# Optimization experiments

Measured on AMD Instinct MI355X. Metric: run time of the kernel, lower is better.

The kernel has to match this reference:

```python
import jax, jax.numpy as jnp
import numpy as np

H = 16  # num_heads


def setup_inputs() -> dict:
    key = jax.random.key(0)
    ks = jax.random.split(key, 12)
    B, L, E = 2, 2048, 1024
    s = 1.0 / np.sqrt(E)
    inp = {
        "query": jax.random.normal(ks[0], (B, L, E), jnp.float32),
        "key": jax.random.normal(ks[1], (B, L, E), jnp.float32),
        "value": jax.random.normal(ks[2], (B, L, E), jnp.float32),
        "Wq": jax.random.normal(ks[3], (E, E), jnp.float32) * s,
        "bq": jnp.zeros((E,), jnp.float32),
        "Wk": jax.random.normal(ks[4], (E, E), jnp.float32) * s,
        "bk": jnp.zeros((E,), jnp.float32),
        "Wv": jax.random.normal(ks[5], (E, E), jnp.float32) * s,
        "bv": jnp.zeros((E,), jnp.float32),
        "Wo": jax.random.normal(ks[6], (E, E), jnp.float32) * s,
        "bo": jnp.zeros((E,), jnp.float32),
    }
    return inp


def _split_heads(x, h):
    B, L, E = x.shape
    return x.reshape(B, L, h, E // h).transpose(0, 2, 1, 3)  # [B,h,L,d]


def reference(query, key, value, Wq, bq, Wk, bk, Wv, bv, Wo, bo):
    B, L, E = query.shape
    d = E // H
    q = _split_heads(query @ Wq.T + bq, H)
    k = _split_heads(key @ Wk.T + bk, H)
    v = _split_heads(value @ Wv.T + bv, H)
    scores = jnp.einsum("bhqd,bhkd->bhqk", q, k) / jnp.sqrt(jnp.float32(d))
    weights = jax.nn.softmax(scores, axis=-1)  # [B,h,L,L]
    # dropout is identity in eval mode (deterministic reference)
    Z = jnp.einsum("bhqk,bhkd->bhqd", weights, v)
    Z = Z.transpose(0, 2, 1, 3).reshape(B, L, E)
    out = Z @ Wo.T + bo
    return out, weights
```

## Files before the change

kernel.cpp:

```cpp
#include <hip/hip_runtime.h>

typedef _Float16 half8 __attribute__((ext_vector_type(8)));
typedef float floatx4 __attribute__((ext_vector_type(4)));

__device__ __forceinline__ int lds_off(int row, int chunk) {
    return row * 32 + ((chunk ^ (row & 3)) << 3);
}

template<bool A_F32, bool B_F32, int OUT_MODE>
__global__ __launch_bounds__(256) void gemm128(
    const void* __restrict__ Ap, int lda, long sAz,
    const void* __restrict__ Bp, int ldb, long sBz,
    const float* __restrict__ bias, float scale,
    void* __restrict__ Cp, long sCz, int K)
{
    __shared__ __align__(16) _Float16 sA[128 * 32];
    __shared__ __align__(16) _Float16 sB[128 * 32];

    const int t = threadIdx.x;
    const int tileN = blockIdx.x * 128;
    const int tileM = blockIdx.y * 128;
    const int z = blockIdx.z;

    const int srow = t >> 1, shalf = t & 1, c0 = shalf * 2;
    const int lane = t & 63, wave = t >> 6;
    const int wm = (wave >> 1) * 64, wn = (wave & 1) * 64;
    const int l15 = lane & 15, quad = lane >> 4;

    const char* Abase = (const char*)Ap + (long)z * sAz * (A_F32 ? 4 : 2);
    const char* Bbase = (const char*)Bp + (long)z * sBz * (B_F32 ? 4 : 2);

    floatx4 acc[4][4];
#pragma unroll
    for (int i = 0; i < 4; i++)
#pragma unroll
        for (int j = 0; j < 4; j++)
            acc[i][j] = (floatx4){0.f, 0.f, 0.f, 0.f};

    for (int k0 = 0; k0 < K; k0 += 32) {
        __syncthreads();
        if constexpr (A_F32) {
            const float* src = (const float*)Abase + (long)(tileM + srow) * lda + k0 + shalf * 16;
            float fx[16];
            *(float4*)(fx + 0)  = *(const float4*)(src + 0);
            *(float4*)(fx + 4)  = *(const float4*)(src + 4);
            *(float4*)(fx + 8)  = *(const float4*)(src + 8);
            *(float4*)(fx + 12) = *(const float4*)(src + 12);
            half8 h0, h1;
#pragma unroll
            for (int i = 0; i < 8; i++) { h0[i] = (_Float16)fx[i]; h1[i] = (_Float16)fx[8 + i]; }
            *(half8*)&sA[lds_off(srow, c0)]     = h0;
            *(half8*)&sA[lds_off(srow, c0 + 1)] = h1;
        } else {
            const _Float16* src = (const _Float16*)Abase + (long)(tileM + srow) * lda + k0 + shalf * 16;
            *(half8*)&sA[lds_off(srow, c0)]     = *(const half8*)(src);
            *(half8*)&sA[lds_off(srow, c0 + 1)] = *(const half8*)(src + 8);
        }
        if constexpr (B_F32) {
            const float* src = (const float*)Bbase + (long)(tileN + srow) * ldb + k0 + shalf * 16;
            float fx[16];
            *(float4*)(fx + 0)  = *(const float4*)(src + 0);
            *(float4*)(fx + 4)  = *(const float4*)(src + 4);
            *(float4*)(fx + 8)  = *(const float4*)(src + 8);
            *(float4*)(fx + 12) = *(const float4*)(src + 12);
            half8 h0, h1;
#pragma unroll
            for (int i = 0; i < 8; i++) { h0[i] = (_Float16)fx[i]; h1[i] = (_Float16)fx[8 + i]; }
            *(half8*)&sB[lds_off(srow, c0)]     = h0;
            *(half8*)&sB[lds_off(srow, c0 + 1)] = h1;
        } else {
            const _Float16* src = (const _Float16*)Bbase + (long)(tileN + srow) * ldb + k0 + shalf * 16;
            *(half8*)&sB[lds_off(srow, c0)]     = *(const half8*)(src);
            *(half8*)&sB[lds_off(srow, c0 + 1)] = *(const half8*)(src + 8);
        }
        __syncthreads();

        half8 af[4], bf[4];
#pragma unroll
        for (int i = 0; i < 4; i++) af[i] = *(const half8*)&sA[lds_off(wm + i * 16 + l15, quad)];
#pragma unroll
        for (int j = 0; j < 4; j++) bf[j] = *(const half8*)&sB[lds_off(wn + j * 16 + l15, quad)];
#pragma unroll
        for (int i = 0; i < 4; i++)
#pragma unroll
            for (int j = 0; j < 4; j++)
                acc[i][j] = __builtin_amdgcn_mfma_f32_16x16x32_f16(af[i], bf[j], acc[i][j], 0, 0, 0);
    }

#pragma unroll
    for (int i = 0; i < 4; i++) {
#pragma unroll
        for (int j = 0; j < 4; j++) {
#pragma unroll
            for (int r = 0; r < 4; r++) {
                const int row = tileM + wm + i * 16 + quad * 4 + r;
                const int col = tileN + wn + j * 16 + l15;
                float v = acc[i][j][r] * scale;
                if (bias) v += bias[col];
                if constexpr (OUT_MODE == 0) {
                    _Float16* dst = (_Float16*)Cp;
                    dst[(long)(((row >> 11) << 4) + (col >> 6)) * 131072 + (long)(row & 2047) * 64 + (col & 63)] = (_Float16)v;
                } else if constexpr (OUT_MODE == 1) {
                    _Float16* dst = (_Float16*)Cp;
                    dst[(long)(((row >> 11) << 4) + (col >> 6)) * 131072 + (long)(col & 63) * 2048 + (row & 2047)] = (_Float16)v;
                } else {
                    float* dst = (float*)Cp;
                    dst[(long)row * 1024 + col] = v;
                }
            }
        }
    }
}

__global__ __launch_bounds__(256, 2) void attn_fused(
    const _Float16* __restrict__ Q,
    const _Float16* __restrict__ K,
    const _Float16* __restrict__ Vt,
    float* __restrict__ W,
    _Float16* __restrict__ Z)
{
    __shared__ __align__(16) _Float16 sK[128 * 64];
    __shared__ __align__(16) _Float16 sV[64 * 128];
    __shared__ __align__(16) _Float16 sP[128 * 128];

    const int t = threadIdx.x;
    const int tileM = blockIdx.x * 128;
    const int bh = blockIdx.y;
    const int lane = t & 63, wave = t >> 6;
    const int l15 = lane & 15, quad = lane >> 4;
    const int wm = wave * 32;

    const _Float16* Qb = Q + (long)bh * 131072;
    const _Float16* Kb = K + (long)bh * 131072;
    const _Float16* Vb = Vt + (long)bh * 131072;
    float* Wb = W + (long)bh * 4194304;

    const int krow = t >> 1, khalf = t & 1;
    const int vrow = t >> 2, vq = t & 3;

    half8 qf[2][2];
#pragma unroll
    for (int i = 0; i < 2; i++)
#pragma unroll
        for (int kk = 0; kk < 2; kk++)
            qf[i][kk] = *(const half8*)(Qb + (long)(tileM + wm + i * 16 + l15) * 64 + kk * 32 + quad * 8);

    float m[2][4], l[2][4];
#pragma unroll
    for (int i = 0; i < 2; i++)
#pragma unroll
        for (int r = 0; r < 4; r++) { m[i][r] = -__builtin_inff(); l[i][r] = 0.f; }

    for (int kv = 0; kv < 2048; kv += 128) {
        __syncthreads();
        {
            const _Float16* src = Kb + (long)(kv + krow) * 64 + khalf * 32;
#pragma unroll
            for (int c = 0; c < 4; c++)
                *(half8*)&sK[krow * 64 + ((((khalf * 4 + c)) ^ (krow & 7)) << 3)] = *(const half8*)(src + c * 8);
        }
        __syncthreads();

        floatx4 acc[2][8];
#pragma unroll
        for (int i = 0; i < 2; i++)
#pragma unroll
            for (int j = 0; j < 8; j++) acc[i][j] = (floatx4){0.f, 0.f, 0.f, 0.f};

#pragma unroll
        for (int kk = 0; kk < 2; kk++) {
#pragma unroll
            for (int j = 0; j < 8; j++) {
                const int row = j * 16 + l15;
                half8 bf = *(const half8*)&sK[row * 64 + (((kk * 4 + quad) ^ (row & 7)) << 3)];
                acc[0][j] = __builtin_amdgcn_mfma_f32_16x16x32_f16(qf[0][kk], bf, acc[0][j], 0, 0, 0);
                acc[1][j] = __builtin_amdgcn_mfma_f32_16x16x32_f16(qf[1][kk], bf, acc[1][j], 0, 0, 0);
            }
        }

#pragma unroll
        for (int i = 0; i < 2; i++)
#pragma unroll
            for (int r = 0; r < 4; r++) {
                float tmax = acc[i][0][r];
#pragma unroll
                for (int j = 1; j < 8; j++) tmax = fmaxf(tmax, acc[i][j][r]);
#pragma unroll
                for (int off = 1; off < 16; off <<= 1) tmax = fmaxf(tmax, __shfl_xor(tmax, off));
                const float mn = fmaxf(m[i][r], tmax * 0.125f);
                const float corr = __expf(m[i][r] - mn);
                float ts = 0.f;
#pragma unroll
                for (int j = 0; j < 8; j++) ts += __expf(acc[i][j][r] * 0.125f - mn);
#pragma unroll
                for (int off = 1; off < 16; off <<= 1) ts += __shfl_xor(ts, off);
                l[i][r] = l[i][r] * corr + ts;
                m[i][r] = mn;
            }
    }

#pragma unroll
    for (int i = 0; i < 2; i++)
#pragma unroll
        for (int r = 0; r < 4; r++) l[i][r] = 1.f / l[i][r];

    floatx4 accz[2][4];
#pragma unroll
    for (int i = 0; i < 2; i++)
#pragma unroll
        for (int j = 0; j < 4; j++) accz[i][j] = (floatx4){0.f, 0.f, 0.f, 0.f};

    for (int kv = 0; kv < 2048; kv += 128) {
        __syncthreads();
        {
            const _Float16* src = Kb + (long)(kv + krow) * 64 + khalf * 32;
#pragma unroll
            for (int c = 0; c < 4; c++)
                *(half8*)&sK[krow * 64 + ((((khalf * 4 + c)) ^ (krow & 7)) << 3)] = *(const half8*)(src + c * 8);
            const _Float16* vsrc = Vb + (long)vrow * 2048 + kv;
#pragma unroll
            for (int c = 0; c < 4; c++) {
                const int ch = vq + c * 4;
                *(half8*)&sV[vrow * 128 + ((ch ^ (vrow & 15)) << 3)] = *(const half8*)(vsrc + ch * 8);
            }
        }
        __syncthreads();

        floatx4 acc[2][8];
#pragma unroll
        for (int i = 0; i < 2; i++)
#pragma unroll
            for (int j = 0; j < 8; j++) acc[i][j] = (floatx4){0.f, 0.f, 0.f, 0.f};

#pragma unroll
        for (int kk = 0; kk < 2; kk++) {
#pragma unroll
            for (int j = 0; j < 8; j++) {
                const int row = j * 16 + l15;
                half8 bf = *(const half8*)&sK[row * 64 + (((kk * 4 + quad) ^ (row & 7)) << 3)];
                acc[0][j] = __builtin_amdgcn_mfma_f32_16x16x32_f16(qf[0][kk], bf, acc[0][j], 0, 0, 0);
                acc[1][j] = __builtin_amdgcn_mfma_f32_16x16x32_f16(qf[1][kk], bf, acc[1][j], 0, 0, 0);
            }
        }

#pragma unroll
        for (int i = 0; i < 2; i++) {
#pragma unroll
            for (int r = 0; r < 4; r++) {
                const int q = wm + i * 16 + quad * 4 + r;
                float* wr = Wb + (long)(tileM + q) * 2048 + kv + l15;
                _Float16* sprow = &sP[q * 128 + (l15 & 7)];
                const int qx = q & 15;
                const int hi = l15 >> 3;
#pragma unroll
                for (int j = 0; j < 8; j++) {
                    const float p = __expf(acc[i][j][r] * 0.125f - m[i][r]) * l[i][r];
                    __builtin_nontemporal_store(p, wr + j * 16);
                    sprow[((j * 2 + hi) ^ qx) << 3] = (_Float16)p;
                }
            }
        }
        __syncthreads();

#pragma unroll
        for (int kk = 0; kk < 4; kk++) {
            half8 pf[2];
#pragma unroll
            for (int i = 0; i < 2; i++) {
                const int q = wm + i * 16 + l15;
                pf[i] = *(const half8*)&sP[q * 128 + (((kk * 4 + quad) ^ (q & 15)) << 3)];
            }
#pragma unroll
            for (int j = 0; j < 4; j++) {
                const int d = j * 16 + l15;
                half8 vf = *(const half8*)&sV[d * 128 + (((kk * 4 + quad) ^ (d & 15)) << 3)];
                accz[0][j] = __builtin_amdgcn_mfma_f32_16x16x32_f16(pf[0], vf, accz[0][j], 0, 0, 0);
                accz[1][j] = __builtin_amdgcn_mfma_f32_16x16x32_f16(pf[1], vf, accz[1][j], 0, 0, 0);
            }
        }
    }

    const int bb = bh >> 4, hd = bh & 15;
#pragma unroll
    for (int i = 0; i < 2; i++)
#pragma unroll
        for (int j = 0; j < 4; j++)
#pragma unroll
            for (int r = 0; r < 4; r++)
                Z[(long)(bb * 2048 + tileM + wm + i * 16 + quad * 4 + r) * 1024 + hd * 64 + j * 16 + l15] =
                    (_Float16)accz[i][j][r];
}

extern "C" void kernel_launch(void* const* d_in, const int* in_sizes, int n_in,
                              void* d_out, int out_size, void* d_ws, size_t ws_size,
                              hipStream_t stream) {
    (void)in_sizes; (void)n_in; (void)out_size; (void)ws_size;
    const float* query = (const float*)d_in[0];
    const float* key   = (const float*)d_in[1];
    const float* value = (const float*)d_in[2];
    const float* Wq = (const float*)d_in[3];
    const float* bq = (const float*)d_in[4];
    const float* Wk = (const float*)d_in[5];
    const float* bk = (const float*)d_in[6];
    const float* Wv = (const float*)d_in[7];
    const float* bv = (const float*)d_in[8];
    const float* Wo = (const float*)d_in[9];
    const float* bo = (const float*)d_in[10];

    _Float16* wsQ  = (_Float16*)d_ws;
    _Float16* wsK  = wsQ + 4194304;
    _Float16* wsVt = wsK + 4194304;
    _Float16* wsZ  = wsVt + 4194304;

    float* outF = (float*)d_out;
    float* Wgt  = outF + 4194304;

    dim3 blk(256);
    gemm128<true, true, 0><<<dim3(8, 32, 1), blk, 0, stream>>>(query, 1024, 0, Wq, 1024, 0, bq, 1.0f, wsQ, 0, 1024);
    gemm128<true, true, 0><<<dim3(8, 32, 1), blk, 0, stream>>>(key,   1024, 0, Wk, 1024, 0, bk, 1.0f, wsK, 0, 1024);
    gemm128<true, true, 1><<<dim3(8, 32, 1), blk, 0, stream>>>(value, 1024, 0, Wv, 1024, 0, bv, 1.0f, wsVt, 0, 1024);
    attn_fused<<<dim3(16, 32), blk, 0, stream>>>(wsQ, wsK, wsVt, Wgt, wsZ);
    gemm128<false, true, 2><<<dim3(8, 32, 1), blk, 0, stream>>>(wsZ, 1024, 0, Wo, 1024, 0, bo, 1.0f, outF, 0, 1024);
}
```

Before: 904.0 us.

## Prefetch next tiles into registers and batch QKV projections into one launch

```diff
diff --git a/kernel.cpp b/kernel.cpp
--- a/kernel.cpp
+++ b/kernel.cpp
@@ -1,18 +1,30 @@
 #include <hip/hip_runtime.h>
 
 typedef _Float16 half8 __attribute__((ext_vector_type(8)));
+typedef _Float16 half4 __attribute__((ext_vector_type(4)));
 typedef float floatx4 __attribute__((ext_vector_type(4)));
 
 __device__ __forceinline__ int lds_off(int row, int chunk) {
     return row * 32 + ((chunk ^ (row & 3)) << 3);
 }
 
-template<bool A_F32, bool B_F32, int OUT_MODE>
-__global__ __launch_bounds__(256) void gemm128(
-    const void* __restrict__ Ap, int lda, long sAz,
-    const void* __restrict__ Bp, int ldb, long sBz,
-    const float* __restrict__ bias, float scale,
-    void* __restrict__ Cp, long sCz, int K)
+__device__ __forceinline__ void ld16f(float* d, const float* s) {
+    *(float4*)(d + 0)  = *(const float4*)(s + 0);
+    *(float4*)(d + 4)  = *(const float4*)(s + 4);
+    *(float4*)(d + 8)  = *(const float4*)(s + 8);
+    *(float4*)(d + 12) = *(const float4*)(s + 12);
+}
+
+__device__ __forceinline__ void cvt16(half8& h0, half8& h1, const float* f) {
+#pragma unroll
+    for (int i = 0; i < 8; i++) { h0[i] = (_Float16)f[i]; h1[i] = (_Float16)f[8 + i]; }
+}
+
+__global__ __launch_bounds__(256) void gemm_qkv(
+    const float* __restrict__ q, const float* __restrict__ k, const float* __restrict__ v,
+    const float* __restrict__ Wq, const float* __restrict__ Wk, const float* __restrict__ Wv,
+    const float* __restrict__ bq, const float* __restrict__ bk, const float* __restrict__ bv,
+    _Float16* __restrict__ outQ, _Float16* __restrict__ outK, _Float16* __restrict__ outVt)
 {
     __shared__ __align__(16) _Float16 sA[128 * 32];
     __shared__ __align__(16) _Float16 sB[128 * 32];
@@ -22,13 +34,21 @@
     const int tileM = blockIdx.y * 128;
     const int z = blockIdx.z;
 
+    const float* Ab = (z == 0) ? q : (z == 1 ? k : v);
+    const float* Bb = (z == 0) ? Wq : (z == 1 ? Wk : Wv);
+    const float* bias = (z == 0) ? bq : (z == 1 ? bk : bv);
+
     const int srow = t >> 1, shalf = t & 1, c0 = shalf * 2;
     const int lane = t & 63, wave = t >> 6;
     const int wm = (wave >> 1) * 64, wn = (wave & 1) * 64;
     const int l15 = lane & 15, quad = lane >> 4;
 
-    const char* Abase = (const char*)Ap + (long)z * sAz * (A_F32 ? 4 : 2);
-    const char* Bbase = (const char*)Bp + (long)z * sBz * (B_F32 ? 4 : 2);
+    const float* Arow = Ab + (long)(tileM + srow) * 1024 + shalf * 16;
+    const float* Brow = Bb + (long)(tileN + srow) * 1024 + shalf * 16;
+
+    float fA[16], fB[16];
+    ld16f(fA, Arow);
+    ld16f(fB, Brow);
 
     floatx4 acc[4][4];
 #pragma unroll
@@ -37,44 +57,23 @@
         for (int j = 0; j < 4; j++)
             acc[i][j] = (floatx4){0.f, 0.f, 0.f, 0.f};
 
-    for (int k0 = 0; k0 < K; k0 += 32) {
-        __syncthreads();
-        if constexpr (A_F32) {
-            const float* src = (const float*)Abase + (long)(tileM + srow) * lda + k0 + shalf * 16;
-            float fx[16];
-            *(float4*)(fx + 0)  = *(const float4*)(src + 0);
-            *(float4*)(fx + 4)  = *(const float4*)(src + 4);
-            *(float4*)(fx + 8)  = *(const float4*)(src + 8);
-            *(float4*)(fx + 12) = *(const float4*)(src + 12);
+    for (int it = 0; it < 32; ++it) {
+        __syncthreads();
+        {
             half8 h0, h1;
-#pragma unroll
-            for (int i = 0; i < 8; i++) { h0[i] = (_Float16)fx[i]; h1[i] = (_Float16)fx[8 + i]; }
+            cvt16(h0, h1, fA);
             *(half8*)&sA[lds_off(srow, c0)]     = h0;
             *(half8*)&sA[lds_off(srow, c0 + 1)] = h1;
-        } else {
-            const _Float16* src = (const _Float16*)Abase + (long)(tileM + srow) * lda + k0 + shalf * 16;
-            *(half8*)&sA[lds_off(srow, c0)]     = *(const half8*)(src);
-            *(half8*)&sA[lds_off(srow, c0 + 1)] = *(const half8*)(src + 8);
-        }
-        if constexpr (B_F32) {
-            const float* src = (const float*)Bbase + (long)(tileN + srow) * ldb + k0 + shalf * 16;
-            float fx[16];
-            *(float4*)(fx + 0)  = *(const float4*)(src + 0);
-            *(float4*)(fx + 4)  = *(const float4*)(src + 4);
-            *(float4*)(fx + 8)  = *(const float4*)(src + 8);
-            *(float4*)(fx + 12) = *(const float4*)(src + 12);
-            half8 h0, h1;
-#pragma unroll
-            for (int i = 0; i < 8; i++) { h0[i] = (_Float16)fx[i]; h1[i] = (_Float16)fx[8 + i]; }
+            cvt16(h0, h1, fB);
             *(half8*)&sB[lds_off(srow, c0)]     = h0;
             *(half8*)&sB[lds_off(srow, c0 + 1)] = h1;
-        } else {
-            const _Float16* src = (const _Float16*)Bbase + (long)(tileN + srow) * ldb + k0 + shalf * 16;
-            *(half8*)&sB[lds_off(srow, c0)]     = *(const half8*)(src);
-            *(half8*)&sB[lds_off(srow, c0 + 1)] = *(const half8*)(src + 8);
-        }
-        __syncthreads();
-
+        }
+        __syncthreads();
+        if (it + 1 < 32) {
+            const int k1 = (it + 1) << 5;
+            ld16f(fA, Arow + k1);
+            ld16f(fB, Brow + k1);
+        }
         half8 af[4], bf[4];
 #pragma unroll
         for (int i = 0; i < 4; i++) af[i] = *(const half8*)&sA[lds_off(wm + i * 16 + l15, quad)];
@@ -91,25 +90,98 @@
     for (int i = 0; i < 4; i++) {
 #pragma unroll
         for (int j = 0; j < 4; j++) {
+            const int row0 = tileM + wm + i * 16 + quad * 4;
+            const int col  = tileN + wn + j * 16 + l15;
+            if (z == 2) {
+                half4 hv;
+#pragma unroll
+                for (int r = 0; r < 4; r++) hv[r] = (_Float16)(acc[i][j][r] + bias[col]);
+                const int bh = ((row0 >> 11) << 4) + (col >> 6);
+                *(half4*)&outVt[(long)bh * 131072 + (long)(col & 63) * 2048 + (row0 & 2047)] = hv;
+            } else {
+                _Float16* dst = z ? outK : outQ;
+#pragma unroll
+                for (int r = 0; r < 4; r++) {
+                    const int row = row0 + r;
+                    dst[(long)(((row >> 11) << 4) + (col >> 6)) * 131072 + (long)(row & 2047) * 64 + (col & 63)] =
+                        (_Float16)(acc[i][j][r] + bias[col]);
+                }
+            }
+        }
+    }
+}
+
+__global__ __launch_bounds__(256) void gemm_out(
+    const _Float16* __restrict__ A, const float* __restrict__ B,
+    const float* __restrict__ bias, float* __restrict__ C)
+{
+    __shared__ __align__(16) _Float16 sA[128 * 32];
+    __shared__ __align__(16) _Float16 sB[128 * 32];
+
+    const int t = threadIdx.x;
+    const int tileN = blockIdx.x * 128;
+    const int tileM = blockIdx.y * 128;
+
+    const int srow = t >> 1, shalf = t & 1, c0 = shalf * 2;
+    const int lane = t & 63, wave = t >> 6;
+    const int wm = (wave >> 1) * 64, wn = (wave & 1) * 64;
+    const int l15 = lane & 15, quad = lane >> 4;
+
+    const _Float16* Arow = A + (long)(tileM + srow) * 1024 + shalf * 16;
+    const float*    Brow = B + (long)(tileN + srow) * 1024 + shalf * 16;
+
+    half8 hA[2];
+    float fB[16];
+    hA[0] = *(const half8*)Arow;
+    hA[1] = *(const half8*)(Arow + 8);
+    ld16f(fB, Brow);
+
+    floatx4 acc[4][4];
+#pragma unroll
+    for (int i = 0; i < 4; i++)
+#pragma unroll
+        for (int j = 0; j < 4; j++)
+            acc[i][j] = (floatx4){0.f, 0.f, 0.f, 0.f};
+
+    for (int it = 0; it < 32; ++it) {
+        __syncthreads();
+        {
+            *(half8*)&sA[lds_off(srow, c0)]     = hA[0];
+            *(half8*)&sA[lds_off(srow, c0 + 1)] = hA[1];
+            half8 h0, h1;
+            cvt16(h0, h1, fB);
+            *(half8*)&sB[lds_off(srow, c0)]     = h0;
+            *(half8*)&sB[lds_off(srow, c0 + 1)] = h1;
+        }
+        __syncthreads();
+        if (it + 1 < 32) {
+            const int k1 = (it + 1) << 5;
+            hA[0] = *(const half8*)(Arow + k1);
+            hA[1] = *(const half8*)(Arow + k1 + 8);
+            ld16f(fB, Brow + k1);
+        }
+        half8 af[4], bf[4];
+#pragma unroll
+        for (int i = 0; i < 4; i++) af[i] = *(const half8*)&sA[lds_off(wm + i * 16 + l15, quad)];
+#pragma unroll
+        for (int j = 0; j < 4; j++) bf[j] = *(const half8*)&sB[lds_off(wn + j * 16 + l15, quad)];
+#pragma unroll
+        for (int i = 0; i < 4; i++)
+#pragma unroll
+            for (int j = 0; j < 4; j++)
+                acc[i][j] = __builtin_amdgcn_mfma_f32_16x16x32_f16(af[i], bf[j], acc[i][j], 0, 0, 0);
+    }
+
+#pragma unroll
+    for (int i = 0; i < 4; i++)
+#pragma unroll
+        for (int j = 0; j < 4; j++)
 #pragma unroll
             for (int r = 0; r < 4; r++) {
                 const int row = tileM + wm + i * 16 + quad * 4 + r;
                 const int col = tileN + wn + j * 16 + l15;
-                float v = acc[i][j][r] * scale;
-                if (bias) v += bias[col];
-                if constexpr (OUT_MODE == 0) {
-                    _Float16* dst = (_Float16*)Cp;
-                    dst[(long)(((row >> 11) << 4) + (col >> 6)) * 131072 + (long)(row & 2047) * 64 + (col & 63)] = (_Float16)v;
-                } else if constexpr (OUT_MODE == 1) {
-                    _Float16* dst = (_Float16*)Cp;
-                    dst[(long)(((row >> 11) << 4) + (col >> 6)) * 131072 + (long)(col & 63) * 2048 + (row & 2047)] = (_Float16)v;
-                } else {
-                    float* dst = (float*)Cp;
-                    dst[(long)row * 1024 + col] = v;
-                }
-            }
-        }
-    }
+                C[(long)row * 1024 + col] = acc[i][j][r] + bias[col];
+            }
 }
 
 __global__ __launch_bounds__(256, 2) void attn_fused(
@@ -151,15 +223,23 @@
 #pragma unroll
         for (int r = 0; r < 4; r++) { m[i][r] = -__builtin_inff(); l[i][r] = 0.f; }
 
+    const _Float16* Ksrc = Kb + (long)krow * 64 + khalf * 32;
+    const _Float16* Vsrc = Vb + (long)vrow * 2048;
+
+    half8 kr[4], vr[4];
+#pragma unroll
+    for (int c = 0; c < 4; c++) kr[c] = *(const half8*)(Ksrc + c * 8);
+
     for (int kv = 0; kv < 2048; kv += 128) {
         __syncthreads();
-        {
-            const _Float16* src = Kb + (long)(kv + krow) * 64 + khalf * 32;
-#pragma unroll
-            for (int c = 0; c < 4; c++)
-                *(half8*)&sK[krow * 64 + ((((khalf * 4 + c)) ^ (krow & 7)) << 3)] = *(const half8*)(src + c * 8);
-        }
-        __syncthreads();
+#pragma unroll
+        for (int c = 0; c < 4; c++)
+            *(half8*)&sK[krow * 64 + (((khalf * 4 + c) ^ (krow & 7)) << 3)] = kr[c];
+        __syncthreads();
+        if (kv + 128 < 2048) {
+#pragma unroll
+            for (int c = 0; c < 4; c++) kr[c] = *(const half8*)(Ksrc + (long)(kv + 128) * 64 + c * 8);
+        }
 
         floatx4 acc[2][8];
 #pragma unroll
@@ -210,21 +290,28 @@
 #pragma unroll
         for (int j = 0; j < 4; j++) accz[i][j] = (floatx4){0.f, 0.f, 0.f, 0.f};
 
+#pragma unroll
+    for (int c = 0; c < 4; c++) kr[c] = *(const half8*)(Ksrc + c * 8);
+#pragma unroll
+    for (int c = 0; c < 4; c++) vr[c] = *(const half8*)(Vsrc + (vq + c * 4) * 8);
+
     for (int kv = 0; kv < 2048; kv += 128) {
         __syncthreads();
-        {
-            const _Float16* src = Kb + (long)(kv + krow) * 64 + khalf * 32;
-#pragma unroll
-            for (int c = 0; c < 4; c++)
-                *(half8*)&sK[krow * 64 + ((((khalf * 4 + c)) ^ (krow & 7)) << 3)] = *(const half8*)(src + c * 8);
-            const _Float16* vsrc = Vb + (long)vrow * 2048 + kv;
-#pragma unroll
-            for (int c = 0; c < 4; c++) {
-                const int ch = vq + c * 4;
-                *(half8*)&sV[vrow * 128 + ((ch ^ (vrow & 15)) << 3)] = *(const half8*)(vsrc + ch * 8);
-            }
-        }
-        __syncthreads();
+#pragma unroll
+        for (int c = 0; c < 4; c++)
+            *(half8*)&sK[krow * 64 + (((khalf * 4 + c) ^ (krow & 7)) << 3)] = kr[c];
+#pragma unroll
+        for (int c = 0; c < 4; c++) {
+            const int ch = vq + c * 4;
+            *(half8*)&sV[vrow * 128 + ((ch ^ (vrow & 15)) << 3)] = vr[c];
+        }
+        __syncthreads();
+        if (kv + 128 < 2048) {
+#pragma unroll
+            for (int c = 0; c < 4; c++) kr[c] = *(const half8*)(Ksrc + (long)(kv + 128) * 64 + c * 8);
+#pragma unroll
+            for (int c = 0; c < 4; c++) vr[c] = *(const half8*)(Vsrc + kv + 128 + (vq + c * 4) * 8);
+        }
 
         floatx4 acc[2][8];
 #pragma unroll
@@ -316,9 +403,7 @@
     float* Wgt  = outF + 4194304;
 
     dim3 blk(256);
-    gemm128<true, true, 0><<<dim3(8, 32, 1), blk, 0, stream>>>(query, 1024, 0, Wq, 1024, 0, bq, 1.0f, wsQ, 0, 1024);
-    gemm128<true, true, 0><<<dim3(8, 32, 1), blk, 0, stream>>>(key,   1024, 0, Wk, 1024, 0, bk, 1.0f, wsK, 0, 1024);
-    gemm128<true, true, 1><<<dim3(8, 32, 1), blk, 0, stream>>>(value, 1024, 0, Wv, 1024, 0, bv, 1.0f, wsVt, 0, 1024);
+    gemm_qkv<<<dim3(8, 32, 3), blk, 0, stream>>>(query, key, value, Wq, Wk, Wv, bq, bk, bv, wsQ, wsK, wsVt);
     attn_fused<<<dim3(16, 32), blk, 0, stream>>>(wsQ, wsK, wsVt, Wgt, wsZ);
-    gemm128<false, true, 2><<<dim3(8, 32, 1), blk, 0, stream>>>(wsZ, 1024, 0, Wo, 1024, 0, bo, 1.0f, outF, 0, 1024);
-}
+    gemm_out<<<dim3(8, 32), blk, 0, stream>>>(wsZ, Wo, bo, outF);
+}
```

Measured after the change: 850.8 us. 5.9% less time.
